# Kernel optimization log

Measured on AMD Instinct MI355X. Metric: run time of the kernel, lower is better.

Reference implementation:

```python
import jax, jax.numpy as jnp
import numpy as np

B, C, H, W = 4, 3, 256, 256
NCC = 64            # num_conv_channels
N_HIDDEN = 20 - 2   # hidden_block applied num_hiddel_blocks-2 times (shared weights)
EPS = 1e-5          # BatchNorm eps (eval mode: running stats; Dropout2d is identity in eval)


def _bayer_mask():
    # RGGB Bayer pattern: each channel sampled only at its sites, zeros elsewhere
    m = np.zeros((3, H, W), dtype=np.float32)
    m[0, 0::2, 0::2] = 1.0  # R
    m[1, 0::2, 1::2] = 1.0  # G
    m[1, 1::2, 0::2] = 1.0  # G
    m[2, 1::2, 1::2] = 1.0  # B
    return jnp.asarray(m)


def setup_inputs() -> dict:
    key = jax.random.key(0)
    ks = jax.random.split(key, 8)
    X = jax.random.uniform(ks[0], (B, C, H, W), dtype=jnp.float32) * _bayer_mask()[None]
    w_in = jax.random.normal(ks[1], (NCC, 3, 3, 3), dtype=jnp.float32) * 0.15
    b_in = jnp.zeros((NCC,), jnp.float32)
    w_h = jax.random.normal(ks[2], (NCC, NCC, 3, 3), dtype=jnp.float32) * 0.04
    b_h = jnp.zeros((NCC,), jnp.float32)
    w_out = jax.random.normal(ks[3], (3, NCC, 3, 3), dtype=jnp.float32) * 0.04
    b_out = jnp.zeros((3,), jnp.float32)
    def bn_params(n):
        return (jnp.ones((n,), jnp.float32), jnp.zeros((n,), jnp.float32),
                jnp.zeros((n,), jnp.float32), jnp.ones((n,), jnp.float32))
    g_in, be_in, m_in, v_in = bn_params(NCC)
    g_h, be_h, m_h, v_h = bn_params(NCC)
    g_out, be_out, m_out, v_out = bn_params(3)
    return dict(X=X, w_in=w_in, b_in=b_in, g_in=g_in, be_in=be_in, m_in=m_in, v_in=v_in,
                w_h=w_h, b_h=b_h, g_h=g_h, be_h=be_h, m_h=m_h, v_h=v_h,
                w_out=w_out, b_out=b_out, g_out=g_out, be_out=be_out, m_out=m_out, v_out=v_out)


def _conv(x, w, b):
    y = jax.lax.conv_general_dilated(x, w, (1, 1), ((1, 1), (1, 1)),
                                     dimension_numbers=('NCHW', 'OIHW', 'NCHW'))
    return y + b[None, :, None, None]


def _bn(x, g, be, m, v):
    scale = (g / jnp.sqrt(v + EPS))[None, :, None, None]
    return (x - m[None, :, None, None]) * scale + be[None, :, None, None]


def _interpolate_zeros(x):
    # Vectorized masked cross-neighbor average at zero sites, dividing by the
    # count of strictly-positive neighbors (zero-padded borders).
    p = jnp.pad(x, ((0, 0), (0, 0), (1, 1), (1, 1)))
    left = p[:, :, 1:-1, :-2]
    right = p[:, :, 1:-1, 2:]
    top = p[:, :, :-2, 1:-1]
    bottom = p[:, :, 2:, 1:-1]
    nb_sum = left + right + top + bottom
    nb_cnt = ((left > 0).astype(x.dtype) + (right > 0).astype(x.dtype)
              + (top > 0).astype(x.dtype) + (bottom > 0).astype(x.dtype))
    mean = jnp.where(nb_cnt > 0, nb_sum / jnp.maximum(nb_cnt, 1.0), 0.0)
    return jnp.where(x == 0, mean, x)


def reference(X, w_in, b_in, g_in, be_in, m_in, v_in,
              w_h, b_h, g_h, be_h, m_h, v_h,
              w_out, b_out, g_out, be_out, m_out, v_out):
    y = jax.nn.selu(_bn(_conv(X, w_in, b_in), g_in, be_in, m_in, v_in))

    def hidden(y, _):
        y = jax.nn.selu(_bn(_conv(y, w_h, b_h), g_h, be_h, m_h, v_h))
        return y, None

    y, _ = jax.lax.scan(hidden, y, None, length=N_HIDDEN)
    y = jax.nn.selu(_bn(_conv(y, w_out, b_out), g_out, be_out, m_out, v_out))
    return y + _interpolate_zeros(X)
```

## Files before the change

kernel.cpp:

```cpp
#include <hip/hip_runtime.h>

#define EPS 1e-5f
#define SELU_L 1.0507009873554805f
#define SELU_A 1.6732632423543772f
#define SELU_LA (SELU_L * SELU_A)

typedef _Float16 half8 __attribute__((ext_vector_type(8)));
typedef _Float16 half4 __attribute__((ext_vector_type(4)));
typedef float floatx4 __attribute__((ext_vector_type(4)));

__device__ __forceinline__ float selu_f(float x) {
    return x > 0.f ? SELU_L * x : SELU_LA * (__expf(x) - 1.f);
}

__device__ __forceinline__ void gload_lds16(const _Float16* g, _Float16* l) {
    __builtin_amdgcn_global_load_lds(
        (const __attribute__((address_space(1))) void*)g,
        (__attribute__((address_space(3))) void*)l, 16, 0, 0);
}

__global__ __launch_bounds__(256) void k_prep(
    const float* __restrict__ w_h, const float* __restrict__ w_in,
    const float* __restrict__ w_out, _Float16* __restrict__ wb_h,
    _Float16* __restrict__ wb_in, _Float16* __restrict__ wb_out,
    _Float16* __restrict__ zp)
{
    int i = blockIdx.x * 256 + threadIdx.x;
    if (i < 256) zp[i] = (_Float16)0.f;
    if (i < 36864) {
        int t = i >> 11;
        int rem = i & 2047;
        int mi = rem >> 9;
        int L = (rem >> 3) & 63;
        int j = i & 7;
        int co = mi * 16 + (L & 15);
        int ci = ((t & 1) << 5) + ((L >> 4) << 3) + j;
        int s = t >> 1;
        wb_h[i] = (_Float16)w_h[(co * 64 + ci) * 9 + s];
    } else if (i < 36864 + 2048) {
        int e = i - 36864;
        int mi = e >> 9;
        int L = (e >> 3) & 63;
        int j = e & 7;
        int co = mi * 16 + (L & 15);
        int k = ((L >> 4) << 3) + j;
        _Float16 val = (_Float16)0.f;
        if (k < 27) {
            int s = k / 3, ci = k - s * 3;
            val = (_Float16)w_in[(co * 3 + ci) * 9 + s];
        }
        wb_in[e] = val;
    } else if (i < 36864 + 2048 + 9216) {
        int e = i - 36864 - 2048;
        int t = e >> 9;
        int L = (e >> 3) & 63;
        int j = e & 7;
        int co = L & 15;
        int ci = ((t & 1) << 5) + ((L >> 4) << 3) + j;
        int s = t >> 1;
        _Float16 val = (_Float16)0.f;
        if (co < 3) val = (_Float16)w_out[(co * 64 + ci) * 9 + s];
        wb_out[e] = val;
    }
}

__global__ __launch_bounds__(256) void k_conv_in_mfma(
    const float* __restrict__ X, const _Float16* __restrict__ wb,
    const float* __restrict__ bconv, const float* __restrict__ g,
    const float* __restrict__ be, const float* __restrict__ bm,
    const float* __restrict__ bv, _Float16* __restrict__ dst)
{
    __shared__ float s_x[3][18][18];
    __shared__ float s_sc[64], s_bs[64];
    const int tid = threadIdx.x;
    const int w0 = blockIdx.x * 16, h0 = blockIdx.y * 16, b = blockIdx.z;

    if (tid < 64) {
        float sc = g[tid] * rsqrtf(bv[tid] + EPS);
        s_sc[tid] = sc;
        s_bs[tid] = (bconv[tid] - bm[tid]) * sc + be[tid];
    }
    for (int idx = tid; idx < 3 * 324; idx += 256) {
        int ci = idx / 324, rem = idx - ci * 324;
        int r = rem / 18, c = rem - r * 18;
        int gh = h0 - 1 + r, gw = w0 - 1 + c;
        float val = 0.f;
        if ((unsigned)gh < 256u && (unsigned)gw < 256u)
            val = X[((b * 3 + ci) << 16) + (gh << 8) + gw];
        s_x[ci][r][c] = val;
    }
    __syncthreads();

    const int wv = tid >> 6, L = tid & 63, quad = L >> 4, l15 = L & 15;
    half8 a[4];
    #pragma unroll
    for (int mi = 0; mi < 4; ++mi)
        a[mi] = *(const half8*)(wb + (mi * 64 + L) * 8);

    floatx4 acc[4][4];
    #pragma unroll
    for (int mi = 0; mi < 4; ++mi)
        #pragma unroll
        for (int ni = 0; ni < 4; ++ni) acc[mi][ni] = (floatx4){0.f, 0.f, 0.f, 0.f};

    #pragma unroll
    for (int ni = 0; ni < 4; ++ni) {
        half8 bfr;
        #pragma unroll
        for (int j = 0; j < 8; ++j) {
            int k = quad * 8 + j;
            float xv = 0.f;
            if (k < 27) {
                int s = k / 3, ci = k - s * 3;
                int kh = s / 3, kw = s - kh * 3;
                xv = s_x[ci][wv * 4 + ni + kh][l15 + kw];
            }
            bfr[j] = (_Float16)xv;
        }
        #pragma unroll
        for (int mi = 0; mi < 4; ++mi)
            acc[mi][ni] = __builtin_amdgcn_mfma_f32_16x16x32_f16(a[mi], bfr, acc[mi][ni], 0, 0, 0);
    }

    _Float16* db = dst + ((size_t)b << 22);
    #pragma unroll
    for (int mi = 0; mi < 4; ++mi) {
        const int cob = mi * 16 + quad * 4;
        floatx4 sc = *(const floatx4*)(&s_sc[cob]);
        floatx4 bs = *(const floatx4*)(&s_bs[cob]);
        #pragma unroll
        for (int ni = 0; ni < 4; ++ni) {
            half4 ov;
            #pragma unroll
            for (int r = 0; r < 4; ++r)
                ov[r] = (_Float16)selu_f(acc[mi][ni][r] * sc[r] + bs[r]);
            const int row = h0 + wv * 4 + ni, col = w0 + l15;
            *(half4*)(db + ((((row << 8) + col) << 6) + cob)) = ov;
        }
    }
}

__global__ __launch_bounds__(1024) void k_hidden_v9(
    const _Float16* __restrict__ src, const _Float16* __restrict__ wb,
    const float* __restrict__ bconv, const float* __restrict__ g,
    const float* __restrict__ be, const float* __restrict__ bm,
    const float* __restrict__ bv, const _Float16* __restrict__ zp,
    _Float16* __restrict__ dst)
{
    __shared__ _Float16 s_w[36864];
    __shared__ _Float16 s_act[2][20992];
    __shared__ float s_sc[64], s_bs[64];
    const int tid = threadIdx.x;
    const int wv = tid >> 6, L = tid & 63, quad = L >> 4, l15 = L & 15;
    const int rh = wv >> 1, mh = wv & 1;

    if (tid < 64) {
        float sc = g[tid] * rsqrtf(bv[tid] + EPS);
        s_sc[tid] = sc;
        s_bs[tid] = (bconv[tid] - bm[tid]) * sc + be[tid];
    }

    #pragma unroll
    for (int k = 0; k < 5; ++k) {
        const int wc = k * 16 + wv;
        if (wc < 72)
            gload_lds16(wb + ((wc << 6) + L) * 8, &s_w[wc << 9]);
    }

    auto stage = [&](int tau, int buf) {
        const int b = tau >> 8, rem = tau & 255;
        const int h0 = (rem >> 4) << 4, w0 = (rem & 15) << 4;
        const _Float16* sb = src + ((size_t)b << 22);
        #pragma unroll
        for (int k = 0; k < 3; ++k) {
            const int wc = k * 16 + wv;
            if (wc < 41) {
                const int p = (wc << 3) + (L >> 3);
                const int sd = (L & 7) ^ (p & 7);
                const int rp = p / 18, cl = p - rp * 18;
                const int gh = h0 - 1 + rp, gw = w0 - 1 + cl;
                const _Float16* gp = (p < 324 && (unsigned)gh < 256u && (unsigned)gw < 256u)
                    ? sb + ((((gh << 8) + gw) << 6) + (sd << 3)) : zp;
                gload_lds16(gp, &s_act[buf][wc << 9]);
            }
        }
    };

    const int tau0 = blockIdx.x << 2;
    stage(tau0, 0);
    __syncthreads();

    for (int ti = 0; ti < 4; ++ti) {
        const int tau = tau0 + ti, cur = ti & 1;
        if (ti < 3) stage(tau + 1, cur ^ 1);

        floatx4 acc[2][2];
        #pragma unroll
        for (int m = 0; m < 2; ++m)
            #pragma unroll
            for (int ni = 0; ni < 2; ++ni) acc[m][ni] = (floatx4){0.f, 0.f, 0.f, 0.f};

        const _Float16* bufp = &s_act[cur][0];
        #pragma unroll
        for (int h = 0; h < 2; ++h) {
            const int sb8 = (h << 2) + quad;
            #pragma unroll
            for (int kw = 0; kw < 3; ++kw) {
                half8 ac[3][2];
                #pragma unroll
                for (int kh = 0; kh < 3; ++kh) {
                    const int t = ((kh * 3 + kw) << 1) + h;
                    ac[kh][0] = *(const half8*)(&s_w[((t * 4 + mh * 2 + 0) * 64 + L) * 8]);
                    ac[kh][1] = *(const half8*)(&s_w[((t * 4 + mh * 2 + 1) * 64 + L) * 8]);
                }
                #pragma unroll
                for (int j = 0; j < 4; ++j) {
                    const int p = (rh * 2 + j) * 18 + l15 + kw;
                    half8 bfr = *(const half8*)(bufp + (p << 6) + (((p & 7) ^ sb8) << 3));
                    #pragma unroll
                    for (int kh = 0; kh < 3; ++kh) {
                        const int ni = j - kh;
                        if (ni >= 0 && ni < 2) {
                            acc[0][ni] = __builtin_amdgcn_mfma_f32_16x16x32_f16(ac[kh][0], bfr, acc[0][ni], 0, 0, 0);
                            acc[1][ni] = __builtin_amdgcn_mfma_f32_16x16x32_f16(ac[kh][1], bfr, acc[1][ni], 0, 0, 0);
                        }
                    }
                }
            }
        }

        const int b = tau >> 8, rem = tau & 255;
        const int h0 = (rem >> 4) << 4, w0 = (rem & 15) << 4;
        _Float16* db = dst + ((size_t)b << 22);
        #pragma unroll
        for (int m = 0; m < 2; ++m) {
            const int cob = (mh * 2 + m) * 16 + quad * 4;
            floatx4 sc = *(const floatx4*)(&s_sc[cob]);
            floatx4 bs = *(const floatx4*)(&s_bs[cob]);
            #pragma unroll
            for (int ni = 0; ni < 2; ++ni) {
                half4 ov;
                #pragma unroll
                for (int r = 0; r < 4; ++r)
                    ov[r] = (_Float16)selu_f(acc[m][ni][r] * sc[r] + bs[r]);
                const int row = h0 + rh * 2 + ni, col = w0 + l15;
                *(half4*)(db + ((((row << 8) + col) << 6) + cob)) = ov;
            }
        }
        __syncthreads();
    }
}

__global__ __launch_bounds__(256) void k_conv_out_mfma(
    const _Float16* __restrict__ src, const _Float16* __restrict__ wb,
    const float* __restrict__ bconv, const float* __restrict__ g,
    const float* __restrict__ be, const float* __restrict__ bm,
    const float* __restrict__ bv, const float* __restrict__ X,
    float* __restrict__ out)
{
    __shared__ _Float16 s_in[324 * 72];
    const int tid = threadIdx.x;
    const int w0 = blockIdx.x * 16, h0 = blockIdx.y * 16, b = blockIdx.z;
    const _Float16* sb = src + ((size_t)b << 22);

    for (int idx = tid; idx < 2592; idx += 256) {
        int r = idx / 144, cpos = idx - r * 144;
        int col = cpos >> 3, sub = cpos & 7;
        int gh = h0 - 1 + r, gw = w0 - 1 + col;
        half8 val = {0, 0, 0, 0, 0, 0, 0, 0};
        if ((unsigned)gh < 256u && (unsigned)gw < 256u)
            val = *(const half8*)(sb + ((((gh << 8) + gw) << 6) + (sub << 3)));
        *(half8*)(&s_in[(r * 18 + col) * 72 + (sub << 3)]) = val;
    }
    __syncthreads();

    const int wv = tid >> 6, L = tid & 63, quad = L >> 4, l15 = L & 15;
    floatx4 acc[4];
    #pragma unroll
    for (int ni = 0; ni < 4; ++ni) acc[ni] = (floatx4){0.f, 0.f, 0.f, 0.f};

    #pragma unroll
    for (int t = 0; t < 18; ++t) {
        const int s = t >> 1, ci0 = (t & 1) << 5;
        const int kh = s / 3, kw = s - kh * 3;
        half8 a = *(const half8*)(wb + (t * 64 + L) * 8);
        #pragma unroll
        for (int ni = 0; ni < 4; ++ni) {
            const int row = wv * 4 + ni + kh, col = l15 + kw;
            half8 bfr = *(const half8*)(&s_in[(row * 18 + col) * 72 + ci0 + quad * 8]);
            acc[ni] = __builtin_amdgcn_mfma_f32_16x16x32_f16(a, bfr, acc[ni], 0, 0, 0);
        }
    }

    if (quad == 0) {
        float sc[3], bs[3];
        #pragma unroll
        for (int co = 0; co < 3; ++co) {
            sc[co] = g[co] * rsqrtf(bv[co] + EPS);
            bs[co] = (bconv[co] - bm[co]) * sc[co] + be[co];
        }
        #pragma unroll
        for (int ni = 0; ni < 4; ++ni) {
            const int h = h0 + wv * 4 + ni, wc = w0 + l15;
            #pragma unroll
            for (int co = 0; co < 3; ++co) {
                float val = selu_f(acc[ni][co] * sc[co] + bs[co]);
                const float* Xc = X + ((size_t)(b * 3 + co) << 16);
                float x = Xc[(h << 8) + wc];
                float res;
                if (x == 0.f) {
                    float lft = (wc > 0)   ? Xc[(h << 8) + wc - 1] : 0.f;
                    float rgt = (wc < 255) ? Xc[(h << 8) + wc + 1] : 0.f;
                    float top = (h > 0)    ? Xc[((h - 1) << 8) + wc] : 0.f;
                    float bot = (h < 255)  ? Xc[((h + 1) << 8) + wc] : 0.f;
                    float sm = lft + rgt + top + bot;
                    int cnt = (lft > 0.f) + (rgt > 0.f) + (top > 0.f) + (bot > 0.f);
                    res = cnt > 0 ? sm / (float)cnt : 0.f;
                } else {
                    res = x;
                }
                out[((b * 3 + co) << 16) + (h << 8) + wc] = val + res;
            }
        }
    }
}

extern "C" void kernel_launch(void* const* d_in, const int* in_sizes, int n_in,
                              void* d_out, int out_size, void* d_ws, size_t ws_size,
                              hipStream_t stream) {
    (void)in_sizes; (void)n_in; (void)out_size; (void)ws_size;
    const float* X    = (const float*)d_in[0];
    const float* w_in = (const float*)d_in[1];
    const float* b_in = (const float*)d_in[2];
    const float* g_in = (const float*)d_in[3];
    const float* be_in= (const float*)d_in[4];
    const float* m_in = (const float*)d_in[5];
    const float* v_in = (const float*)d_in[6];
    const float* w_h  = (const float*)d_in[7];
    const float* b_h  = (const float*)d_in[8];
    const float* g_h  = (const float*)d_in[9];
    const float* be_h = (const float*)d_in[10];
    const float* m_h  = (const float*)d_in[11];
    const float* v_h  = (const float*)d_in[12];
    const float* w_o  = (const float*)d_in[13];
    const float* b_o  = (const float*)d_in[14];
    const float* g_o  = (const float*)d_in[15];
    const float* be_o = (const float*)d_in[16];
    const float* m_o  = (const float*)d_in[17];
    const float* v_o  = (const float*)d_in[18];
    float* out = (float*)d_out;

    _Float16* act0  = (_Float16*)d_ws;
    _Float16* act1  = act0 + ((size_t)1 << 24);
    _Float16* wb_h  = act1 + ((size_t)1 << 24);
    _Float16* wb_in = wb_h + 36864;
    _Float16* wb_out= wb_in + 2048;
    _Float16* zp    = wb_out + 9216;

    dim3 grid(16, 16, 4), block(256);
    k_prep<<<188, 256, 0, stream>>>(w_h, w_in, w_o, wb_h, wb_in, wb_out, zp);
    k_conv_in_mfma<<<grid, block, 0, stream>>>(X, wb_in, b_in, g_in, be_in, m_in, v_in, act0);
    _Float16* src = act0;
    _Float16* dst = act1;
    for (int i = 0; i < 18; ++i) {
        k_hidden_v9<<<256, 1024, 0, stream>>>(src, wb_h, b_h, g_h, be_h, m_h, v_h, zp, dst);
        _Float16* t = src; src = dst; dst = t;
    }
    k_conv_out_mfma<<<grid, block, 0, stream>>>(src, wb_out, b_o, g_o, be_o, m_o, v_o, X, out);
}
```

Before: 594.4 us.

## Remap hidden-conv waves to 4 rows by 16 channels to cut weight loads

Changes the per-wave work split in the hidden conv kernel. Before, each wave computed 2 output rows for 32 output channels; now it computes 4 rows for 16 channels. Each wave loads half as many weight fragments and reuses each one over more rows, but reads 6 activation rows per kw instead of 4. The total MFMA count is unchanged, so the aim is to reduce LDS traffic per MFMA and shift the balance between weight and activation reads.

```diff
diff --git a/kernel.cpp b/kernel.cpp
--- a/kernel.cpp
+++ b/kernel.cpp
@@ -140,7 +140,7 @@
     }
 }
 
-__global__ __launch_bounds__(1024) void k_hidden_v9(
+__global__ __launch_bounds__(1024) void k_hidden_v13(
     const _Float16* __restrict__ src, const _Float16* __restrict__ wb,
     const float* __restrict__ bconv, const float* __restrict__ g,
     const float* __restrict__ be, const float* __restrict__ bm,
@@ -152,7 +152,7 @@
     __shared__ float s_sc[64], s_bs[64];
     const int tid = threadIdx.x;
     const int wv = tid >> 6, L = tid & 63, quad = L >> 4, l15 = L & 15;
-    const int rh = wv >> 1, mh = wv & 1;
+    const int rq = wv >> 2, mq = wv & 3;
 
     if (tid < 64) {
         float sc = g[tid] * rsqrtf(bv[tid] + EPS);
@@ -194,11 +194,9 @@
         const int tau = tau0 + ti, cur = ti & 1;
         if (ti < 3) stage(tau + 1, cur ^ 1);
 
-        floatx4 acc[2][2];
-        #pragma unroll
-        for (int m = 0; m < 2; ++m)
-            #pragma unroll
-            for (int ni = 0; ni < 2; ++ni) acc[m][ni] = (floatx4){0.f, 0.f, 0.f, 0.f};
+        floatx4 acc[4];
+        #pragma unroll
+        for (int ni = 0; ni < 4; ++ni) acc[ni] = (floatx4){0.f, 0.f, 0.f, 0.f};
 
         const _Float16* bufp = &s_act[cur][0];
         #pragma unroll
@@ -206,24 +204,21 @@
             const int sb8 = (h << 2) + quad;
             #pragma unroll
             for (int kw = 0; kw < 3; ++kw) {
-                half8 ac[3][2];
+                half8 ac[3];
                 #pragma unroll
                 for (int kh = 0; kh < 3; ++kh) {
                     const int t = ((kh * 3 + kw) << 1) + h;
-                    ac[kh][0] = *(const half8*)(&s_w[((t * 4 + mh * 2 + 0) * 64 + L) * 8]);
-                    ac[kh][1] = *(const half8*)(&s_w[((t * 4 + mh * 2 + 1) * 64 + L) * 8]);
+                    ac[kh] = *(const half8*)(&s_w[((t * 4 + mq) * 64 + L) * 8]);
                 }
                 #pragma unroll
-                for (int j = 0; j < 4; ++j) {
-                    const int p = (rh * 2 + j) * 18 + l15 + kw;
+                for (int j = 0; j < 6; ++j) {
+                    const int p = (rq * 4 + j) * 18 + l15 + kw;
                     half8 bfr = *(const half8*)(bufp + (p << 6) + (((p & 7) ^ sb8) << 3));
                     #pragma unroll
                     for (int kh = 0; kh < 3; ++kh) {
                         const int ni = j - kh;
-                        if (ni >= 0 && ni < 2) {
-                            acc[0][ni] = __builtin_amdgcn_mfma_f32_16x16x32_f16(ac[kh][0], bfr, acc[0][ni], 0, 0, 0);
-                            acc[1][ni] = __builtin_amdgcn_mfma_f32_16x16x32_f16(ac[kh][1], bfr, acc[1][ni], 0, 0, 0);
-                        }
+                        if (ni >= 0 && ni < 4)
+                            acc[ni] = __builtin_amdgcn_mfma_f32_16x16x32_f16(ac[kh], bfr, acc[ni], 0, 0, 0);
                     }
                 }
             }
@@ -232,20 +227,17 @@
         const int b = tau >> 8, rem = tau & 255;
         const int h0 = (rem >> 4) << 4, w0 = (rem & 15) << 4;
         _Float16* db = dst + ((size_t)b << 22);
-        #pragma unroll
-        for (int m = 0; m < 2; ++m) {
-            const int cob = (mh * 2 + m) * 16 + quad * 4;
-            floatx4 sc = *(const floatx4*)(&s_sc[cob]);
-            floatx4 bs = *(const floatx4*)(&s_bs[cob]);
+        const int cob = mq * 16 + quad * 4;
+        floatx4 sc = *(const floatx4*)(&s_sc[cob]);
+        floatx4 bs = *(const floatx4*)(&s_bs[cob]);
+        #pragma unroll
+        for (int ni = 0; ni < 4; ++ni) {
+            half4 ov;
             #pragma unroll
-            for (int ni = 0; ni < 2; ++ni) {
-                half4 ov;
-                #pragma unroll
-                for (int r = 0; r < 4; ++r)
-                    ov[r] = (_Float16)selu_f(acc[m][ni][r] * sc[r] + bs[r]);
-                const int row = h0 + rh * 2 + ni, col = w0 + l15;
-                *(half4*)(db + ((((row << 8) + col) << 6) + cob)) = ov;
-            }
+            for (int r = 0; r < 4; ++r)
+                ov[r] = (_Float16)selu_f(acc[ni][r] * sc[r] + bs[r]);
+            const int row = h0 + rq * 4 + ni, col = w0 + l15;
+            *(half4*)(db + ((((row << 8) + col) << 6) + cob)) = ov;
         }
         __syncthreads();
     }
@@ -363,7 +355,7 @@
     _Float16* src = act0;
     _Float16* dst = act1;
     for (int i = 0; i < 18; ++i) {
-        k_hidden_v9<<<256, 1024, 0, stream>>>(src, wb_h, b_h, g_h, be_h, m_h, v_h, zp, dst);
+        k_hidden_v13<<<256, 1024, 0, stream>>>(src, wb_h, b_h, g_h, be_h, m_h, v_h, zp, dst);
         _Float16* t = src; src = dst; dst = t;
     }
     k_conv_out_mfma<<<grid, block, 0, stream>>>(src, wb_out, b_o, g_o, be_o, m_o, v_o, X, out);
```

Measured after the change: 597.9 us. No clear change (+0.6%).
